# Kernel tuning notes

Measured on AMD Instinct MI355X. Metric: run time of the kernel, lower is better.

Reference implementation:

```python
import jax, jax.numpy as jnp
import numpy as np

B, S, D, H = 2, 1536, 1024, 16
DK = D // H
NEG = -1e9
WEIGHT = 1.0  # undefined global `Weight` in source; treated as scalar 1.0


def setup_inputs() -> dict:
    key = jax.random.key(0)
    ks = jax.random.split(key, 16)
    inp = {
        "query": jax.random.normal(ks[0], (B, S, D), jnp.float32),
        "key": jax.random.normal(ks[1], (B, S, D), jnp.float32),
        "value": jax.random.normal(ks[2], (B, S, D), jnp.float32),
        "mask": jax.random.randint(ks[3], (B, 1, 1, S), 0, 2, jnp.int32),
        "mask1": jax.random.randint(ks[4], (B, 1, S, S), 0, 2, jnp.int32).astype(jnp.float32),
        "Wq": jax.random.normal(ks[5], (D, D), jnp.float32) / np.sqrt(D),
        "bq": jnp.zeros((D,), jnp.float32),
        "Wk": jax.random.normal(ks[6], (D, D), jnp.float32) / np.sqrt(D),
        "bk": jnp.zeros((D,), jnp.float32),
        "Wv": jax.random.normal(ks[7], (D, D), jnp.float32) / np.sqrt(D),
        "bv": jnp.zeros((D,), jnp.float32),
        "Wo": jax.random.normal(ks[8], (D, D), jnp.float32) / np.sqrt(D),
        "bo": jnp.zeros((D,), jnp.float32),
    }
    return inp


def _split_heads(x):
    # [B,S,D] -> [B,H,S,DK]
    return x.reshape(B, S, H, DK).transpose(0, 2, 1, 3)


def reference(query, key, value, mask, mask1, Wq, bq, Wk, bk, Wv, bv, Wo, bo):
    q = _split_heads(query @ Wq.T + bq)
    k = _split_heads(key @ Wk.T + bk)
    v = _split_heads(value @ Wv.T + bv)

    scores = jnp.einsum("bhqd,bhkd->bhqk", q, k) / jnp.sqrt(jnp.float32(DK))
    # softmax of mask1 over the query axis (dim=-2), zeros masked out
    m1 = jnp.where(mask1 == 0, NEG, mask1)
    m1s = jax.nn.softmax(m1, axis=-2)
    scores = (1.0 + m1s * mask1) * scores * WEIGHT
    scores = jnp.where(mask == 0, NEG, scores)
    p = jax.nn.softmax(scores, axis=-1)  # dropout: eval mode (identity)
    x = jnp.einsum("bhqk,bhkd->bhqd", p, v)
    x = x.transpose(0, 2, 1, 3).reshape(B, S, D)
    ret = x @ Wo.T + bo
    return ret, scores
```

## Files before the change

kernel.cpp:

```cpp
#include <hip/hip_runtime.h>
#include <hip/hip_bf16.h>

#define B_ 2
#define S_ 1536
#define D_ 1024
#define H_ 16
#define DK_ 64
#define KW_ 48
#define NT_ 24

#define RET_ELEMS 3145728
#define BITPACK_BLOCKS 18432
#define QKV_BLOCKS 768

typedef __attribute__((ext_vector_type(8))) short short8;
typedef __attribute__((ext_vector_type(8))) unsigned short ushort8v;
typedef __attribute__((ext_vector_type(4))) unsigned short ushort4v;
typedef __attribute__((ext_vector_type(4))) float f32x4;

__device__ __forceinline__ unsigned short bf16_rne(float f) {
    return __builtin_bit_cast(unsigned short, __float2bfloat16(f));
}

struct CvtJobs {
    const float* src[7];
    unsigned short* dst[7];
};

__global__ __launch_bounds__(256) void preproc_kernel(
    const float* __restrict__ mask1, unsigned int* __restrict__ bits,
    float* __restrict__ colsum, CvtJobs j)
{
    const int blk = blockIdx.x;
    if (blk < BITPACK_BLOCKS) {
        if (blk < 12) colsum[blk * 256 + threadIdx.x] = 0.f;
        const size_t gid = (size_t)blk * 256 + threadIdx.x;
        const float v = mask1[gid];
        const unsigned long long bal = __ballot(v != 0.f);
        const int l = threadIdx.x & 63;
        if (l == 0)       bits[gid >> 5] = (unsigned int)bal;
        else if (l == 32) bits[gid >> 5] = (unsigned int)(bal >> 32);
        return;
    }
    int rb = blk - BITPACK_BLOCKS;
    int job, base;
    if (rb < 4608) { job = rb / 1536; base = rb % 1536; }
    else { rb -= 4608; job = 3 + rb / 512; base = rb % 512; }
    const size_t i = ((size_t)base * 256 + threadIdx.x) * 8;
    const float* s = j.src[job] + i;
    float4 f0 = *(const float4*)s;
    float4 f1 = *(const float4*)(s + 4);
    ushort8v u;
    u[0]=bf16_rne(f0.x); u[1]=bf16_rne(f0.y); u[2]=bf16_rne(f0.z); u[3]=bf16_rne(f0.w);
    u[4]=bf16_rne(f1.x); u[5]=bf16_rne(f1.y); u[6]=bf16_rne(f1.z); u[7]=bf16_rne(f1.w);
    *(ushort8v*)(j.dst[job] + i) = u;
}

struct Proj { const unsigned short* A; const unsigned short* W; const float* bias; unsigned short* C; };

__global__ __launch_bounds__(384) void qkv_gemm_kernel(
    Proj p0, Proj p1, Proj p2,
    const unsigned int* __restrict__ bits, float* __restrict__ colsum)
{
    const int bid = blockIdx.x;
    const int tid = threadIdx.x;

    if (bid >= QKV_BLOCKS) {
        const int id2 = bid - QKV_BLOCKS;
        const int b = id2 / 96, rest = id2 % 96;
        const int q0 = (rest >> 2) * 64;
        const int col = (rest & 3) * 384 + tid;
        const int wword = col >> 5, bit = col & 31;
        const unsigned int* p = bits + ((size_t)b * S_ + q0) * KW_ + wword;
        int s = 0;
        #pragma unroll 8
        for (int q = 0; q < 64; ++q) s += (p[(size_t)q * KW_] >> bit) & 1u;
        atomicAdd(&colsum[b * S_ + col], (float)s);
        return;
    }

    const int xcd = bid & 7, idx = bid >> 3;
    const int zm = xcd * 12 + (idx >> 3);
    const int bx = idx & 7;
    const int z = zm / 32, by = zm % 32;

    const unsigned short* A = z == 0 ? p0.A    : (z == 1 ? p1.A    : p2.A);
    const unsigned short* W = z == 0 ? p0.W    : (z == 1 ? p1.W    : p2.W);
    const float* bias       = z == 0 ? p0.bias : (z == 1 ? p1.bias : p2.bias);
    unsigned short* C       = z == 0 ? p0.C    : (z == 1 ? p1.C    : p2.C);

    __shared__ unsigned short As[96][72];
    __shared__ unsigned short Bs[128][72];
    const int w = tid >> 6, lane = tid & 63;
    const int g = lane >> 4, c = lane & 15;
    const int wm = w >> 1, wn = w & 1;
    const int m0 = by * 96, n0 = bx * 128;
    const int trowA = tid >> 2;
    const int tcolA = (tid & 3) * 16;

    f32x4 acc[2][4];
    #pragma unroll
    for (int m = 0; m < 2; ++m)
        #pragma unroll
        for (int n = 0; n < 4; ++n)
            acc[m][n] = f32x4{0.f, 0.f, 0.f, 0.f};

    for (int k0 = 0; k0 < D_; k0 += 64) {
        {
            const unsigned short* ap = A + (size_t)(m0 + trowA) * D_ + k0 + tcolA;
            *(ushort8v*)&As[trowA][tcolA]     = *(const ushort8v*)ap;
            *(ushort8v*)&As[trowA][tcolA + 8] = *(const ushort8v*)(ap + 8);
            const int r1 = tid >> 2, c1 = (tid & 3) * 16;
            const unsigned short* wp = W + (size_t)(n0 + r1) * D_ + k0 + c1;
            *(ushort8v*)&Bs[r1][c1]     = *(const ushort8v*)wp;
            *(ushort8v*)&Bs[r1][c1 + 8] = *(const ushort8v*)(wp + 8);
            if (tid < 128) {
                const int c2i = 384 + tid;
                const int r2 = c2i >> 2, c2 = (c2i & 3) * 16;
                const unsigned short* wp2 = W + (size_t)(n0 + r2) * D_ + k0 + c2;
                *(ushort8v*)&Bs[r2][c2]     = *(const ushort8v*)wp2;
                *(ushort8v*)&Bs[r2][c2 + 8] = *(const ushort8v*)(wp2 + 8);
            }
        }
        __syncthreads();
        #pragma unroll
        for (int kk = 0; kk < 2; ++kk) {
            short8 a[2], bb[4];
            #pragma unroll
            for (int m = 0; m < 2; ++m) a[m]  = *(const short8*)&As[wm * 32 + m * 16 + c][kk * 32 + g * 8];
            #pragma unroll
            for (int n = 0; n < 4; ++n) bb[n] = *(const short8*)&Bs[wn * 64 + n * 16 + c][kk * 32 + g * 8];
            __builtin_amdgcn_s_setprio(1);
            #pragma unroll
            for (int m = 0; m < 2; ++m)
                #pragma unroll
                for (int n = 0; n < 4; ++n)
                    acc[m][n] = __builtin_amdgcn_mfma_f32_16x16x32_bf16(a[m], bb[n], acc[m][n], 0, 0, 0);
            __builtin_amdgcn_s_setprio(0);
        }
        __syncthreads();
    }
    #pragma unroll
    for (int n = 0; n < 4; ++n) {
        const int col = n0 + wn * 64 + n * 16 + c;
        const float bval = bias[col];
        #pragma unroll
        for (int m = 0; m < 2; ++m) {
            const int row0 = m0 + wm * 32 + m * 16 + g * 4;
            #pragma unroll
            for (int r = 0; r < 4; ++r)
                C[(size_t)(row0 + r) * D_ + col] = bf16_rne(acc[m][n][r] + bval);
        }
    }
}

__global__ __launch_bounds__(256) void out_gemm_kernel(
    const unsigned short* __restrict__ A, const unsigned short* __restrict__ W,
    const float* __restrict__ bias, float* __restrict__ C)
{
    const int bid = blockIdx.x;
    const int xcd = bid & 7, idx = bid >> 3;
    const int yg = xcd * 6 + (idx >> 4);
    const int bx = idx & 15;

    __shared__ unsigned short As[64][72];
    __shared__ unsigned short Bs[64][72];
    const int tid = threadIdx.x;
    const int w = tid >> 6, lane = tid & 63;
    const int g = lane >> 4, c = lane & 15;
    const int wm = w >> 1, wn = w & 1;
    const int m0 = yg * 64, n0 = bx * 64;
    const int trow = tid >> 2;
    const int tcol = (tid & 3) * 16;

    f32x4 acc[2][2];
    #pragma unroll
    for (int m = 0; m < 2; ++m)
        #pragma unroll
        for (int n = 0; n < 2; ++n)
            acc[m][n] = f32x4{0.f, 0.f, 0.f, 0.f};

    for (int k0 = 0; k0 < D_; k0 += 64) {
        {
            const unsigned short* ap = A + (size_t)(m0 + trow) * D_ + k0 + tcol;
            *(ushort8v*)&As[trow][tcol]     = *(const ushort8v*)ap;
            *(ushort8v*)&As[trow][tcol + 8] = *(const ushort8v*)(ap + 8);
            const unsigned short* wp = W + (size_t)(n0 + trow) * D_ + k0 + tcol;
            *(ushort8v*)&Bs[trow][tcol]     = *(const ushort8v*)wp;
            *(ushort8v*)&Bs[trow][tcol + 8] = *(const ushort8v*)(wp + 8);
        }
        __syncthreads();
        #pragma unroll
        for (int kk = 0; kk < 2; ++kk) {
            short8 a[2], bb[2];
            #pragma unroll
            for (int m = 0; m < 2; ++m) a[m]  = *(const short8*)&As[wm * 32 + m * 16 + c][kk * 32 + g * 8];
            #pragma unroll
            for (int n = 0; n < 2; ++n) bb[n] = *(const short8*)&Bs[wn * 32 + n * 16 + c][kk * 32 + g * 8];
            __builtin_amdgcn_s_setprio(1);
            #pragma unroll
            for (int m = 0; m < 2; ++m)
                #pragma unroll
                for (int n = 0; n < 2; ++n)
                    acc[m][n] = __builtin_amdgcn_mfma_f32_16x16x32_bf16(a[m], bb[n], acc[m][n], 0, 0, 0);
            __builtin_amdgcn_s_setprio(0);
        }
        __syncthreads();
    }
    #pragma unroll
    for (int n = 0; n < 2; ++n) {
        const int col = n0 + wn * 32 + n * 16 + c;
        const float bval = bias[col];
        #pragma unroll
        for (int m = 0; m < 2; ++m) {
            const int row0 = m0 + wm * 32 + m * 16 + g * 4;
            #pragma unroll
            for (int r = 0; r < 4; ++r)
                C[(size_t)(row0 + r) * D_ + col] = acc[m][n][r] + bval;
        }
    }
}

__global__ __launch_bounds__(256) void attn_kernel(
    const unsigned short* __restrict__ Qb, const unsigned short* __restrict__ Kb,
    const unsigned short* __restrict__ Vb, const int* __restrict__ mask,
    const unsigned int* __restrict__ bits, const float* __restrict__ colsum,
    float* __restrict__ scores, unsigned short* __restrict__ X)
{
    const int bid = blockIdx.x;
    const int xcd = bid & 7, idx = bid >> 3;
    const int grp = xcd * 4 + idx / 24;
    const int qt  = idx % 24;
    const int h = grp & 15, b = grp >> 4;

    const int tid = threadIdx.x;
    const int w = tid >> 6, lane = tid & 63;
    const int g = lane >> 4, c = lane & 15;

    __shared__ unsigned short VT_lds[2][64][72];
    __shared__ unsigned short P_lds[4][16][72];
    __shared__ float fac_lds[S_];

    for (int i = tid; i < S_; i += 256) {
        const int km = mask[b * S_ + i];
        const float cnt = colsum[b * S_ + i];
        fac_lds[i] = (km == 0) ? -1.f : ((cnt > 0.f) ? (1.f / cnt) : 0.f);
    }

    const int qrow0 = qt * 64 + w * 16;
    const unsigned short* qptr = Qb + ((size_t)b * S_ + qrow0 + c) * D_ + h * DK_;
    const short8 qf0 = *(const short8*)(qptr + g * 8);
    const short8 qf1 = *(const short8*)(qptr + 32 + g * 8);

    float mrow = -INFINITY, lrow = 0.f;
    f32x4 o[4];
    #pragma unroll
    for (int n = 0; n < 4; ++n) o[n] = f32x4{0.f, 0.f, 0.f, 0.f};

    float* srow = scores + ((((size_t)(b * H_ + h)) * S_ + qrow0 + c) * S_);
    const unsigned int* brow = bits + ((size_t)b * S_ + qrow0 + c) * KW_;
    const int kr = tid & 63, half = tid >> 6;
    const unsigned short* vrow = Vb + ((size_t)b * S_ + kr) * D_ + h * DK_ + half * 16;

    {
        short8 v0 = *(const short8*)vrow;
        short8 v1 = *(const short8*)(vrow + 8);
        #pragma unroll
        for (int j = 0; j < 8; ++j) {
            VT_lds[0][half * 16 + j][kr]     = (unsigned short)v0[j];
            VT_lds[0][half * 16 + 8 + j][kr] = (unsigned short)v1[j];
        }
    }
    __syncthreads();

    for (int kt = 0; kt < NT_; ++kt) {
        const int k0 = kt * 64;
        const int cur = kt & 1;
        const bool have_next = (kt + 1) < NT_;

        short8 nv0, nv1;
        if (have_next) {
            const unsigned short* vs = vrow + (size_t)(k0 + 64) * D_;
            nv0 = *(const short8*)vs;
            nv1 = *(const short8*)(vs + 8);
        }

        f32x4 sacc[4];
        #pragma unroll
        for (int n = 0; n < 4; ++n) sacc[n] = f32x4{0.f, 0.f, 0.f, 0.f};
        short8 kf0[4], kf1[4];
        #pragma unroll
        for (int n = 0; n < 4; ++n) {
            const unsigned short* kp = Kb + ((size_t)b * S_ + k0 + n * 16 + c) * D_ + h * DK_;
            kf0[n] = *(const short8*)(kp + g * 8);
            kf1[n] = *(const short8*)(kp + 32 + g * 8);
        }
        __builtin_amdgcn_s_setprio(1);
        #pragma unroll
        for (int n = 0; n < 4; ++n) {
            sacc[n] = __builtin_amdgcn_mfma_f32_16x16x32_bf16(kf0[n], qf0, sacc[n], 0, 0, 0);
            sacc[n] = __builtin_amdgcn_mfma_f32_16x16x32_bf16(kf1[n], qf1, sacc[n], 0, 0, 0);
        }
        __builtin_amdgcn_s_setprio(0);

        const unsigned int w0 = brow[(k0 >> 5)];
        const unsigned int w1 = brow[(k0 >> 5) + 1];
        float pmax = -INFINITY;
        f32x4 sv[4];
        #pragma unroll
        for (int n = 0; n < 4; ++n) {
            const f32x4 fv = *(const f32x4*)&fac_lds[k0 + n * 16 + g * 4];
            const unsigned int wsel = (n < 2) ? w0 : w1;
            #pragma unroll
            for (int r = 0; r < 4; ++r) {
                const int kl = n * 16 + g * 4 + r;
                const float f = fv[r];
                const float icnt = fmaxf(f, 0.f);
                const float bit = (float)((wsel >> (kl & 31)) & 1u);
                float s = sacc[n][r] * 0.125f * (1.f + bit * icnt);
                s = (f < 0.f) ? -1e9f : s;
                sv[n][r] = s;
                pmax = fmaxf(pmax, s);
            }
            __builtin_nontemporal_store(sv[n], (f32x4*)&srow[k0 + n * 16 + g * 4]);
        }

        pmax = fmaxf(pmax, __shfl_xor(pmax, 16));
        pmax = fmaxf(pmax, __shfl_xor(pmax, 32));
        const float nm = fmaxf(mrow, pmax);
        const float scq = __expf(mrow - nm);
        mrow = nm;
        lrow *= scq;
        float sc_o[4];
        #pragma unroll
        for (int r = 0; r < 4; ++r) sc_o[r] = __shfl(scq, (lane & 48) | (g * 4 + r));
        #pragma unroll
        for (int n = 0; n < 4; ++n)
            #pragma unroll
            for (int r = 0; r < 4; ++r) o[n][r] *= sc_o[r];

        #pragma unroll
        for (int n = 0; n < 4; ++n) {
            ushort4v pu;
            #pragma unroll
            for (int r = 0; r < 4; ++r) {
                const float p = __expf(sv[n][r] - mrow);
                lrow += p;
                pu[r] = bf16_rne(p);
            }
            *(ushort4v*)&P_lds[w][c][n * 16 + g * 4] = pu;
        }

        if (have_next) {
            #pragma unroll
            for (int j = 0; j < 8; ++j) {
                VT_lds[cur ^ 1][half * 16 + j][kr]     = (unsigned short)nv0[j];
                VT_lds[cur ^ 1][half * 16 + 8 + j][kr] = (unsigned short)nv1[j];
            }
        }

        __builtin_amdgcn_s_setprio(1);
        #pragma unroll
        for (int kk = 0; kk < 2; ++kk) {
            const short8 pa = *(const short8*)&P_lds[w][c][kk * 32 + g * 8];
            #pragma unroll
            for (int n = 0; n < 4; ++n) {
                const short8 vf = *(const short8*)&VT_lds[cur][n * 16 + c][kk * 32 + g * 8];
                o[n] = __builtin_amdgcn_mfma_f32_16x16x32_bf16(pa, vf, o[n], 0, 0, 0);
            }
        }
        __builtin_amdgcn_s_setprio(0);
        __syncthreads();
    }

    lrow += __shfl_xor(lrow, 16);
    lrow += __shfl_xor(lrow, 32);
    const float linv = 1.f / lrow;
    float linv_o[4];
    #pragma unroll
    for (int r = 0; r < 4; ++r) linv_o[r] = __shfl(linv, (lane & 48) | (g * 4 + r));
    #pragma unroll
    for (int n = 0; n < 4; ++n)
        #pragma unroll
        for (int r = 0; r < 4; ++r) {
            const size_t idx2 = ((size_t)b * S_ + qrow0 + g * 4 + r) * D_ + h * DK_ + n * 16 + c;
            X[idx2] = bf16_rne(o[n][r] * linv_o[r]);
        }
}

extern "C" void kernel_launch(void* const* d_in, const int* in_sizes, int n_in,
                              void* d_out, int out_size, void* d_ws, size_t ws_size,
                              hipStream_t stream) {
    const float* query = (const float*)d_in[0];
    const float* key   = (const float*)d_in[1];
    const float* value = (const float*)d_in[2];
    const int*   mask  = (const int*)d_in[3];
    const float* mask1 = (const float*)d_in[4];
    const float* Wq = (const float*)d_in[5];
    const float* bq = (const float*)d_in[6];
    const float* Wk = (const float*)d_in[7];
    const float* bk = (const float*)d_in[8];
    const float* Wv = (const float*)d_in[9];
    const float* bv = (const float*)d_in[10];
    const float* Wo = (const float*)d_in[11];
    const float* bo = (const float*)d_in[12];

    float* ret_out    = (float*)d_out;
    float* scores_out = ret_out + RET_ELEMS;

    const size_t SZ = (size_t)B_ * S_ * D_;
    const size_t WZ = (size_t)D_ * D_;
    float* colsum = (float*)d_ws;
    unsigned int* bits = (unsigned int*)((char*)d_ws + 16384);
    unsigned short* Qb  = (unsigned short*)((char*)d_ws + 16384 + 589824);
    unsigned short* Kb  = Qb + SZ;
    unsigned short* Vb  = Kb + SZ;
    unsigned short* Xb  = Vb + SZ;
    unsigned short* qf  = Xb + SZ;
    unsigned short* kf  = qf + SZ;
    unsigned short* vf  = kf + SZ;
    unsigned short* Wqb = vf + SZ;
    unsigned short* Wkb = Wqb + WZ;
    unsigned short* Wvb = Wkb + WZ;
    unsigned short* Wob = Wvb + WZ;

    CvtJobs jobs;
    jobs.src[0] = query; jobs.dst[0] = qf;
    jobs.src[1] = key;   jobs.dst[1] = kf;
    jobs.src[2] = value; jobs.dst[2] = vf;
    jobs.src[3] = Wq;    jobs.dst[3] = Wqb;
    jobs.src[4] = Wk;    jobs.dst[4] = Wkb;
    jobs.src[5] = Wv;    jobs.dst[5] = Wvb;
    jobs.src[6] = Wo;    jobs.dst[6] = Wob;

    preproc_kernel<<<BITPACK_BLOCKS + 3 * 1536 + 4 * 512, 256, 0, stream>>>(mask1, bits, colsum, jobs);

    Proj p0{qf, Wqb, bq, Qb}, p1{kf, Wkb, bk, Kb}, p2{vf, Wvb, bv, Vb};
    qkv_gemm_kernel<<<QKV_BLOCKS + 192, 384, 0, stream>>>(p0, p1, p2, bits, colsum);

    attn_kernel<<<768, 256, 0, stream>>>(Qb, Kb, Vb, mask, bits, colsum, scores_out, Xb);

    out_gemm_kernel<<<768, 256, 0, stream>>>(Xb, Wob, bo, ret_out);
}
```

Baseline: 204.5 us.

## Split attention key loop across two half-blocks and merge softmax states

The attention kernel now launches 512 threads per block. Two groups of four waves each process half of the key tiles for the same 64 query rows, and their running max, sum and output are merged through shared memory at the end. This halves the serial key-tile loop per wave and doubles the waves in flight, to better hide the latency of the large scores stores and the K/V loads. In exchange, the V tile is no longer double-buffered: it is written after a barrier, which adds a second barrier per iteration. There is also an extra LDS merge step and higher per-block resource use.

```diff
diff --git a/kernel.cpp b/kernel.cpp
--- a/kernel.cpp
+++ b/kernel.cpp
@@ -8,6 +8,7 @@
 #define DK_ 64
 #define KW_ 48
 #define NT_ 24
+#define NTH_ 12
 
 #define RET_ELEMS 3145728
 #define BITPACK_BLOCKS 18432
@@ -221,7 +222,7 @@
     }
 }
 
-__global__ __launch_bounds__(256) void attn_kernel(
+__global__ __launch_bounds__(512) void attn_kernel(
     const unsigned short* __restrict__ Qb, const unsigned short* __restrict__ Kb,
     const unsigned short* __restrict__ Vb, const int* __restrict__ mask,
     const unsigned int* __restrict__ bits, const float* __restrict__ colsum,
@@ -236,18 +237,19 @@
     const int tid = threadIdx.x;
     const int w = tid >> 6, lane = tid & 63;
     const int g = lane >> 4, c = lane & 15;
+    const int qw = w & 3, half = w >> 2;
 
     __shared__ unsigned short VT_lds[2][64][72];
-    __shared__ unsigned short P_lds[4][16][72];
+    __shared__ unsigned short P_lds[8][16][72];
     __shared__ float fac_lds[S_];
 
-    for (int i = tid; i < S_; i += 256) {
+    for (int i = tid; i < S_; i += 512) {
         const int km = mask[b * S_ + i];
         const float cnt = colsum[b * S_ + i];
         fac_lds[i] = (km == 0) ? -1.f : ((cnt > 0.f) ? (1.f / cnt) : 0.f);
     }
 
-    const int qrow0 = qt * 64 + w * 16;
+    const int qrow0 = qt * 64 + qw * 16;
     const unsigned short* qptr = Qb + ((size_t)b * S_ + qrow0 + c) * D_ + h * DK_;
     const short8 qf0 = *(const short8*)(qptr + g * 8);
     const short8 qf1 = *(const short8*)(qptr + 32 + g * 8);
@@ -259,24 +261,27 @@
 
     float* srow = scores + ((((size_t)(b * H_ + h)) * S_ + qrow0 + c) * S_);
     const unsigned int* brow = bits + ((size_t)b * S_ + qrow0 + c) * KW_;
-    const int kr = tid & 63, half = tid >> 6;
-    const unsigned short* vrow = Vb + ((size_t)b * S_ + kr) * D_ + h * DK_ + half * 16;
+
+    const int tl = tid & 255;
+    const int kr = tl & 63, dkc = tl >> 6;
+    const unsigned short* vrow = Vb + ((size_t)b * S_ + kr) * D_ + h * DK_ + dkc * 16;
+    const int tbase = half * NTH_;
 
     {
-        short8 v0 = *(const short8*)vrow;
-        short8 v1 = *(const short8*)(vrow + 8);
+        const unsigned short* vs = vrow + (size_t)(tbase * 64) * D_;
+        short8 v0 = *(const short8*)vs;
+        short8 v1 = *(const short8*)(vs + 8);
         #pragma unroll
         for (int j = 0; j < 8; ++j) {
-            VT_lds[0][half * 16 + j][kr]     = (unsigned short)v0[j];
-            VT_lds[0][half * 16 + 8 + j][kr] = (unsigned short)v1[j];
+            VT_lds[half][dkc * 16 + j][kr]     = (unsigned short)v0[j];
+            VT_lds[half][dkc * 16 + 8 + j][kr] = (unsigned short)v1[j];
         }
     }
     __syncthreads();
 
-    for (int kt = 0; kt < NT_; ++kt) {
-        const int k0 = kt * 64;
-        const int cur = kt & 1;
-        const bool have_next = (kt + 1) < NT_;
+    for (int t = 0; t < NTH_; ++t) {
+        const int k0 = (tbase + t) * 64;
+        const bool have_next = (t + 1) < NTH_;
 
         short8 nv0, nv1;
         if (have_next) {
@@ -313,10 +318,10 @@
             const unsigned int wsel = (n < 2) ? w0 : w1;
             #pragma unroll
             for (int r = 0; r < 4; ++r) {
-                const int kl = n * 16 + g * 4 + r;
+                const int kl = (n * 16 + g * 4 + r) & 31;
                 const float f = fv[r];
                 const float icnt = fmaxf(f, 0.f);
-                const float bit = (float)((wsel >> (kl & 31)) & 1u);
+                const float bit = (float)((wsel >> kl) & 1u);
                 float s = sacc[n][r] * 0.125f * (1.f + bit * icnt);
                 s = (f < 0.f) ? -1e9f : s;
                 sv[n][r] = s;
@@ -351,41 +356,68 @@
             *(ushort4v*)&P_lds[w][c][n * 16 + g * 4] = pu;
         }
 
-        if (have_next) {
-            #pragma unroll
-            for (int j = 0; j < 8; ++j) {
-                VT_lds[cur ^ 1][half * 16 + j][kr]     = (unsigned short)nv0[j];
-                VT_lds[cur ^ 1][half * 16 + 8 + j][kr] = (unsigned short)nv1[j];
-            }
-        }
-
         __builtin_amdgcn_s_setprio(1);
         #pragma unroll
         for (int kk = 0; kk < 2; ++kk) {
             const short8 pa = *(const short8*)&P_lds[w][c][kk * 32 + g * 8];
             #pragma unroll
             for (int n = 0; n < 4; ++n) {
-                const short8 vf = *(const short8*)&VT_lds[cur][n * 16 + c][kk * 32 + g * 8];
+                const short8 vf = *(const short8*)&VT_lds[half][n * 16 + c][kk * 32 + g * 8];
                 o[n] = __builtin_amdgcn_mfma_f32_16x16x32_bf16(pa, vf, o[n], 0, 0, 0);
             }
         }
         __builtin_amdgcn_s_setprio(0);
         __syncthreads();
+
+        if (have_next) {
+            #pragma unroll
+            for (int j = 0; j < 8; ++j) {
+                VT_lds[half][dkc * 16 + j][kr]     = (unsigned short)nv0[j];
+                VT_lds[half][dkc * 16 + 8 + j][kr] = (unsigned short)nv1[j];
+            }
+            __syncthreads();
+        }
     }
 
     lrow += __shfl_xor(lrow, 16);
     lrow += __shfl_xor(lrow, 32);
-    const float linv = 1.f / lrow;
-    float linv_o[4];
-    #pragma unroll
-    for (int r = 0; r < 4; ++r) linv_o[r] = __shfl(linv, (lane & 48) | (g * 4 + r));
-    #pragma unroll
-    for (int n = 0; n < 4; ++n)
+
+    float* mo = (float*)P_lds;
+    float* ml = (float*)fac_lds;
+    if (half == 1) {
+        const int base = (qw * 64 + lane) * 16;
+        #pragma unroll
+        for (int n = 0; n < 4; ++n)
+            #pragma unroll
+            for (int r = 0; r < 4; ++r) mo[base + n * 4 + r] = o[n][r];
+        ml[(qw * 64 + lane) * 2 + 0] = mrow;
+        ml[(qw * 64 + lane) * 2 + 1] = lrow;
+    }
+    __syncthreads();
+    if (half == 0) {
+        const int base = (qw * 64 + lane) * 16;
+        const float mB = ml[(qw * 64 + lane) * 2 + 0];
+        const float lB = ml[(qw * 64 + lane) * 2 + 1];
+        const float ms = fmaxf(mrow, mB);
+        const float eA = __expf(mrow - ms);
+        const float eB = __expf(mB - ms);
+        const float linv = 1.f / (lrow * eA + lB * eB);
+        const float fA = eA * linv, fB = eB * linv;
+        float fA_o[4], fB_o[4];
         #pragma unroll
         for (int r = 0; r < 4; ++r) {
-            const size_t idx2 = ((size_t)b * S_ + qrow0 + g * 4 + r) * D_ + h * DK_ + n * 16 + c;
-            X[idx2] = bf16_rne(o[n][r] * linv_o[r]);
-        }
+            fA_o[r] = __shfl(fA, (lane & 48) | (g * 4 + r));
+            fB_o[r] = __shfl(fB, (lane & 48) | (g * 4 + r));
+        }
+        #pragma unroll
+        for (int n = 0; n < 4; ++n)
+            #pragma unroll
+            for (int r = 0; r < 4; ++r) {
+                const float val = o[n][r] * fA_o[r] + mo[base + n * 4 + r] * fB_o[r];
+                const size_t idx2 = ((size_t)b * S_ + qrow0 + g * 4 + r) * D_ + h * DK_ + n * 16 + c;
+                X[idx2] = bf16_rne(val);
+            }
+    }
 }
 
 extern "C" void kernel_launch(void* const* d_in, const int* in_sizes, int n_in,
@@ -438,7 +470,7 @@
     Proj p0{qf, Wqb, bq, Qb}, p1{kf, Wkb, bk, Kb}, p2{vf, Wvb, bv, Vb};
     qkv_gemm_kernel<<<QKV_BLOCKS + 192, 384, 0, stream>>>(p0, p1, p2, bits, colsum);
 
-    attn_kernel<<<768, 256, 0, stream>>>(Qb, Kb, Vb, mask, bits, colsum, scores_out, Xb);
+    attn_kernel<<<768, 512, 0, stream>>>(Qb, Kb, Vb, mask, bits, colsum, scores_out, Xb);
 
     out_gemm_kernel<<<768, 256, 0, stream>>>(Xb, Wob, bo, ret_out);
 }
```

Result: slower. 214.8 us (+5.0%).
